# Optimization experiments

Measured on AMD Instinct MI355X. Metric: run time of the kernel, lower is better.

Reference implementation:

```python
import jax, jax.numpy as jnp
import numpy as np

B, S, D, H = 4, 2048, 1024, 16
DK = D // H


def setup_inputs() -> dict:
    key = jax.random.key(0)
    ks = jax.random.split(key, 5)
    init_std = np.sqrt(2.0 / (D + D))  # trunc bound proxy; plain randn clamped below
    trunc = 3 * init_std

    def w(k):
        return jnp.clip(jax.random.normal(k, (D, D), dtype=jnp.float32), -trunc, trunc)

    x = jax.random.normal(ks[0], (B, S, D), dtype=jnp.float32)
    return {
        "x": x,
        "W_Q": w(ks[1]),
        "W_K": w(ks[2]),
        "W_V": w(ks[3]),
        "W_O": w(ks[4]),
        "is_causal": 1,
    }


def reference(x, W_Q, W_K, W_V, W_O, is_causal):
    b, s, d = x.shape
    # Linear: y = W @ x with W:[out,in], x:[..., in]
    def proj(W, t):
        y = jnp.einsum("oi,bsi->bso", W, t)
        # [b, s, h*dk] -> [b, h, s, dk]
        return y.reshape(b, s, H, DK).transpose(0, 2, 1, 3)

    q = proj(W_Q, x)
    k = proj(W_K, x)
    v = proj(W_V, x)

    scores = jnp.einsum("bhqd,bhkd->bhqk", q, k) * (DK ** -0.5)
    if is_causal:
        causal = jnp.tril(jnp.ones((s, s), dtype=bool))
        scores = jnp.where(causal, scores, -jnp.inf)
    attn = jax.nn.softmax(scores, axis=-1)
    out = jnp.einsum("bhqk,bhkd->bhqd", attn, v)
    out = out.transpose(0, 2, 1, 3).reshape(b, s, H * DK)
    return jnp.einsum("oi,bsi->bso", W_O, out)
```

## Files before the change

### kernel.cpp

```cpp
#include <hip/hip_runtime.h>
#include <stdint.h>

#define NB 4
#define NS 2048
#define ND 1024
#define NH 16
#define NDK 64
#define L2E 1.44269504088896340736f
#define AS1 __attribute__((address_space(1)))
#define AS3 __attribute__((address_space(3)))

typedef __attribute__((ext_vector_type(8)))  short     s16x8;
typedef __attribute__((ext_vector_type(4)))  float     f32x4;
typedef __attribute__((ext_vector_type(16))) float     f32x16;
typedef __attribute__((ext_vector_type(4)))  unsigned  u32x4;

__device__ __forceinline__ unsigned short f2bf(float f) {
    union { float f; unsigned u; } v; v.f = f;
    unsigned r = v.u + 0x7FFFu + ((v.u >> 16) & 1u);
    return (unsigned short)(r >> 16);
}
__device__ __forceinline__ unsigned cvt_pk_bf16(float lo, float hi) {
    unsigned r;
    asm("v_cvt_pk_bf16_f32 %0, %1, %2" : "=v"(r) : "v"(lo), "v"(hi));
    return r;
}
__device__ __forceinline__ void pl32swap(unsigned &a, unsigned &b) {
    asm volatile("v_permlane32_swap_b32 %0, %1" : "+v"(a), "+v"(b));
}
__device__ __forceinline__ float exp2_hw(float x) {
    float r; asm("v_exp_f32 %0, %1" : "=v"(r) : "v"(x)); return r;
}
__device__ __forceinline__ f32x16 fz16() {
    f32x16 z;
#pragma unroll
    for (int r = 0; r < 16; ++r) z[r] = 0.f;
    return z;
}
__device__ __forceinline__ f32x16 mfma32(const s16x8& a, const s16x8& b, const f32x16& c) {
    return __builtin_amdgcn_mfma_f32_32x32x16_bf16(a, b, c, 0, 0, 0);
}

__global__ void detect_dtype(const unsigned* __restrict__ x, int* __restrict__ flag) {
    int lane = threadIdx.x;
    int cnt = 0;
    for (int i = lane; i < 1024; i += 64) {
        unsigned lo = x[i] & 0xFFFFu;
        unsigned e  = (lo >> 7) & 0xFFu;
        cnt += (e >= 100u && e <= 140u) ? 1 : 0;
    }
    for (int d = 1; d < 64; d <<= 1) cnt += __shfl_xor(cnt, d);
    if (lane == 0) flag[0] = (cnt > 512) ? 1 : 0;
}

__global__ void convert_all(const void* __restrict__ x,  const void* __restrict__ wq,
                            const void* __restrict__ wk, const void* __restrict__ wv,
                            unsigned short* __restrict__ XB, unsigned short* __restrict__ WQKV,
                            const int* __restrict__ flagp) {
    const int A  = (NB * NS * ND) / 8;
    const int WC = (ND * ND) / 8;
    int fl = *flagp;
    int i = blockIdx.x * blockDim.x + threadIdx.x;
    int stride = gridDim.x * blockDim.x;
    int total = A + 3 * WC;
    for (; i < total; i += stride) {
        const void* src; unsigned short* dst; long o8;
        if (i < A) { src = x; dst = XB; o8 = i; }
        else {
            int k = i - A, which = k >> 17, o = k & (WC - 1);
            src = which == 0 ? wq : (which == 1 ? wk : wv);
            dst = WQKV + (long)which * (ND * ND);
            o8 = o;
        }
        u32x4 v;
        if (fl) {
            v = *(const u32x4*)((const unsigned short*)src + o8 * 8);
        } else {
            const float* p = (const float*)src + o8 * 8;
            f32x4 a = *(const f32x4*)p;
            f32x4 b = *(const f32x4*)(p + 4);
            v[0] = cvt_pk_bf16(a[0], a[1]);
            v[1] = cvt_pk_bf16(a[2], a[3]);
            v[2] = cvt_pk_bf16(b[0], b[1]);
            v[3] = cvt_pk_bf16(b[2], b[3]);
        }
        *(u32x4*)(dst + o8 * 8) = v;
    }
}

__global__ void convert_bf16(const void* __restrict__ src, unsigned short* __restrict__ dst,
                             int n8, const int* __restrict__ flagp) {
    int i = blockIdx.x * blockDim.x + threadIdx.x;
    int stride = gridDim.x * blockDim.x;
    int fl = *flagp;
    for (; i < n8; i += stride) {
        u32x4 v;
        if (fl) {
            v = *(const u32x4*)((const unsigned short*)src + (long)i * 8);
        } else {
            const float* p = (const float*)src + (long)i * 8;
            f32x4 a = *(const f32x4*)p;
            f32x4 b = *(const f32x4*)(p + 4);
            v[0] = cvt_pk_bf16(a[0], a[1]);
            v[1] = cvt_pk_bf16(a[2], a[3]);
            v[2] = cvt_pk_bf16(b[0], b[1]);
            v[3] = cvt_pk_bf16(b[2], b[3]);
        }
        *(u32x4*)(dst + (long)i * 8) = v;
    }
}

__device__ __forceinline__ void stage_glds64(const unsigned short* __restrict__ src, int ld,
                                             long r0, int k0, unsigned short* lds, int tid) {
#pragma unroll
    for (int h = 0; h < 4; ++h) {
        int c = h * 256 + tid;
        int row = c >> 3;
        int scol = (c & 7) ^ (row & 7);
        const unsigned short* gp = src + (r0 + row) * ld + k0 + scol * 8;
        unsigned short* lp = lds + (c & ~63) * 8;
        __builtin_amdgcn_global_load_lds(
            (const AS1 unsigned short*)gp, (AS3 unsigned short*)lp, 16, 0, 0);
    }
}

template<int OUT_MODE, int NXB>
__global__ __launch_bounds__(256, 2)
void gemm3(const unsigned short* __restrict__ A, const unsigned short* __restrict__ W,
           void* __restrict__ dst, const int* __restrict__ flagp, float scale)
{
    __shared__ unsigned short As[128 * 64];
    __shared__ unsigned short Bs[128 * 64];
    const long TOKc = (long)NB * NS * ND;
    int tid  = threadIdx.x;
    int w    = tid >> 6, lane = tid & 63;
    int wr   = w >> 1,   wc   = w & 1;
    int nwg = (int)(gridDim.x * gridDim.y);
    int bid = (int)(blockIdx.y * gridDim.x + blockIdx.x);
    int nb  = (bid & 7) * (nwg >> 3) + (bid >> 3);
    int n0  = (nb % NXB) * 128;
    long m0 = (long)(nb / NXB) * 128;
    int fl  = *flagp;

    f32x4 zero4 = {0.f, 0.f, 0.f, 0.f};
    f32x4 acc[4][4];
#pragma unroll
    for (int i = 0; i < 4; ++i)
#pragma unroll
        for (int j = 0; j < 4; ++j) acc[i][j] = zero4;

    int lr = lane & 15, lg = lane >> 4;

    for (int k0 = 0; k0 < 1024; k0 += 64) {
        __syncthreads();
        stage_glds64(A, 1024, m0, k0, As, tid);
        stage_glds64(W, 1024, n0, k0, Bs, tid);
        __syncthreads();
#pragma unroll
        for (int kk = 0; kk < 2; ++kk) {
            s16x8 af[4], bf[4];
#pragma unroll
            for (int i = 0; i < 4; ++i) {
                int row = wr * 64 + i * 16 + lr;
                int u = (kk * 4 + lg) ^ (lr & 7);
                af[i] = *(const s16x8*)(As + row * 64 + u * 8);
            }
#pragma unroll
            for (int j = 0; j < 4; ++j) {
                int row = wc * 64 + j * 16 + lr;
                int u = (kk * 4 + lg) ^ (lr & 7);
                bf[j] = *(const s16x8*)(Bs + row * 64 + u * 8);
            }
#pragma unroll
            for (int i = 0; i < 4; ++i)
#pragma unroll
                for (int j = 0; j < 4; ++j)
                    acc[i][j] = __builtin_amdgcn_mfma_f32_16x16x32_bf16(af[i], bf[j], acc[i][j], 0, 0, 0);
        }
    }

    int rbase = (lane >> 4) * 4;
#pragma unroll
    for (int i = 0; i < 4; ++i)
#pragma unroll
        for (int j = 0; j < 4; ++j)
#pragma unroll
            for (int r = 0; r < 4; ++r) {
                long m = m0 + wr * 64 + i * 16 + rbase + r;
                int  n = n0 + wc * 64 + j * 16 + lr;
                float v = acc[i][j][r];
                if (OUT_MODE == 3) {
                    long b = m >> 11, s = m & 2047;
                    int hh = (n >> 6) & 15, dk = n & 63;
                    float sc = (n < 1024) ? scale : 1.0f;
                    long off = (n >= 1024) ? TOKc : 0;
                    ((unsigned short*)dst)[off + (((b * NH + hh) * NS) + s) * NDK + dk] = f2bf(v * sc);
                } else if (OUT_MODE == 1) {
                    int hh = (int)(m >> 6), dk = (int)(m & 63);
                    long b = n >> 11, s = n & 2047;
                    ((unsigned short*)dst)[(((b * NH + hh) * NDK) + dk) * NS + s] = f2bf(v * scale);
                } else {
                    if (fl) ((unsigned short*)dst)[m * 1024 + n] = f2bf(v * scale);
                    else    ((float*)dst)[m * 1024 + n] = v * scale;
                }
            }
}

__device__ __forceinline__ void stage_tile64(const char* __restrict__ srcbase, int rowstride,
                                             unsigned short* lds, int tid) {
#pragma unroll
    for (int h = 0; h < 2; ++h) {
        int c = h * 256 + tid;
        int L = c * 16;
        int row = L >> 7;
        int sr  = (L & 127) ^ ((row & 7) << 4);
        const char* gp = srcbase + row * rowstride + sr;
        unsigned short* lp = lds + (c & ~63) * 8;
        __builtin_amdgcn_global_load_lds((const AS1 unsigned short*)gp,
                                         (AS3 unsigned short*)lp, 16, 0, 0);
    }
}

__device__ __forceinline__ void sm64s(f32x16& st0, f32x16& st1, float& l,
                                      bool mask, int kv0, int qb, int l31, int hi,
                                      s16x8* pf)
{
    if (mask) {
        int q = qb + l31;
#pragma unroll
        for (int r = 0; r < 16; ++r) {
            int crow = (r & 3) + 8 * (r >> 2) + 4 * hi;
            if (kv0 + crow > q)      st0[r] = -1e30f;
            if (kv0 + 32 + crow > q) st1[r] = -1e30f;
        }
    }
#pragma unroll
    for (int r = 0; r < 16; ++r) {
        st0[r] = exp2_hw(st0[r]);
        st1[r] = exp2_hw(st1[r]);
    }
    float s8[8];
#pragma unroll
    for (int r = 0; r < 8; ++r) s8[r] = (st0[r] + st0[r + 8]) + (st1[r] + st1[r + 8]);
    float s4[4];
#pragma unroll
    for (int r = 0; r < 4; ++r) s4[r] = s8[r] + s8[r + 4];
    l += (s4[0] + s4[1]) + (s4[2] + s4[3]);

#pragma unroll
    for (int half = 0; half < 2; ++half) {
        const f32x16& st = half ? st1 : st0;
        unsigned b0 = cvt_pk_bf16(st[0],  st[1]);
        unsigned b1 = cvt_pk_bf16(st[2],  st[3]);
        unsigned b2 = cvt_pk_bf16(st[4],  st[5]);
        unsigned b3 = cvt_pk_bf16(st[6],  st[7]);
        unsigned b4 = cvt_pk_bf16(st[8],  st[9]);
        unsigned b5 = cvt_pk_bf16(st[10], st[11]);
        unsigned b6 = cvt_pk_bf16(st[12], st[13]);
        unsigned b7 = cvt_pk_bf16(st[14], st[15]);
        pl32swap(b0, b2);  pl32swap(b1, b3);
        pl32swap(b4, b6);  pl32swap(b5, b7);
        union { unsigned u[4]; s16x8 v; } p0, p1;
        p0.u[0] = b0; p0.u[1] = b1; p0.u[2] = b2; p0.u[3] = b3;
        p1.u[0] = b4; p1.u[1] = b5; p1.u[2] = b6; p1.u[3] = b7;
        pf[half * 2]     = p0.v;
        pf[half * 2 + 1] = p1.v;
    }
}

__device__ __forceinline__ void attn_epi(unsigned short* epb, const f32x16& o0, const f32x16& o1,
                                         float lrow, int l31, int hi, int lane,
                                         unsigned short* __restrict__ Oo, int qb, int b, int hh)
{
    float lt = lrow + __shfl_xor(lrow, 32);
    float inv = 1.0f / lt;
#pragma unroll
    for (int j = 0; j < 2; ++j) {
        const f32x16& o = j ? o1 : o0;
#pragma unroll
        for (int g = 0; g < 4; ++g) {
            int d0 = j * 32 + g * 8 + hi * 4;
            unsigned lo = cvt_pk_bf16(o[g * 4 + 0] * inv, o[g * 4 + 1] * inv);
            unsigned hw = cvt_pk_bf16(o[g * 4 + 2] * inv, o[g * 4 + 3] * inv);
            unsigned short* p = epb + l31 * 72 + d0;
            *(unsigned*)(p)     = lo;
            *(unsigned*)(p + 2) = hw;
        }
    }
    asm volatile("s_waitcnt lgkmcnt(0)" ::: "memory");
    __builtin_amdgcn_sched_barrier(0);
#pragma unroll
    for (int rr = 0; rr < 4; ++rr) {
        int q2 = rr * 8 + (lane >> 3);
        int d2 = (lane & 7) * 8;
        u32x4 vv = *(const u32x4*)(epb + q2 * 72 + d2);
        *(u32x4*)(Oo + (((long)b * NS + qb + q2) * ND) + hh * NDK + d2) = vv;
    }
}

__global__ __launch_bounds__(256, 3)
void attn_fwd11(const unsigned short* __restrict__ Q,
                const unsigned short* __restrict__ Kt,
                const unsigned short* __restrict__ Vt,
                unsigned short* __restrict__ Oo,
                const int* __restrict__ causalp)
{
    __shared__ char lds[2][16384];
    int tid = threadIdx.x, w = tid >> 6, lane = tid & 63;
    int l31 = lane & 31, hi = lane >> 5;
    int bh = blockIdx.x;
    int j  = 15 - (int)blockIdx.y;
    int t  = 4 * j + w, qb = t * 32;
    int causal = *causalp;
    int nst   = causal ? (2 * j + 2) : (NS / 64);
    int sdiag = causal ? (t >> 1) : 0x7FFFFFFF;

    const unsigned short* Qh = Q  + bh * (NS * NDK);
    const char* Khb = (const char*)(Kt + (long)bh * NS * NDK);
    const char* Vhb = (const char*)(Vt + (long)bh * NDK * NS);

    s16x8 qf[4];
#pragma unroll
    for (int kd = 0; kd < 4; ++kd)
        qf[kd] = *(const s16x8*)(Qh + (qb + l31) * NDK + kd * 16 + hi * 8);

    int koff[4];
#pragma unroll
    for (int kd = 0; kd < 4; ++kd)
        koff[kd] = l31 * 128 + ((kd * 32 + hi * 16) ^ ((l31 & 7) << 4));

    const f32x16 Z16 = fz16();
    f32x16 o0 = fz16(), o1 = fz16();
    float l = 0.f;

    stage_tile64(Khb, 128, (unsigned short*)&lds[0][0], tid);
    stage_tile64(Vhb, NS * 2, (unsigned short*)&lds[0][8192], tid);
    __syncthreads();

    int cur = 0;
    for (int s = 0; s < nst; ++s) {
        if (s + 1 < nst) {
            int kv1 = (s + 1) * 64;
            stage_tile64(Khb + (long)kv1 * 128, 128, (unsigned short*)&lds[cur ^ 1][0], tid);
            stage_tile64(Vhb + kv1 * 2, NS * 2, (unsigned short*)&lds[cur ^ 1][8192], tid);
        }
        if (s <= sdiag) {
            const char* kb = &lds[cur][0];
            const char* vb = &lds[cur][8192];
            f32x16 st0, st1;
            __builtin_amdgcn_s_setprio(1);
            {
                s16x8 k0 = *(const s16x8*)(kb + koff[0]);
                s16x8 k1 = *(const s16x8*)(kb + 4096 + koff[0]);
                st0 = mfma32(k0, qf[0], Z16);
                st1 = mfma32(k1, qf[0], Z16);
            }
#pragma unroll
            for (int kd = 1; kd < 4; ++kd) {
                s16x8 k0 = *(const s16x8*)(kb + koff[kd]);
                s16x8 k1 = *(const s16x8*)(kb + 4096 + koff[kd]);
                st0 = mfma32(k0, qf[kd], st0);
                st1 = mfma32(k1, qf[kd], st1);
            }
            __builtin_amdgcn_s_setprio(0);
            s16x8 pf[4];
            sm64s(st0, st1, l, s == sdiag, s * 64, qb, l31, hi, pf);
            __builtin_amdgcn_s_setprio(1);
#pragma unroll
            for (int ks = 0; ks < 4; ++ks) {
                s16x8 va = *(const s16x8*)(vb + koff[ks]);
                s16x8 wb = *(const s16x8*)(vb + 4096 + koff[ks]);
                o0 = mfma32(va, pf[ks], o0);
                o1 = mfma32(wb, pf[ks], o1);
            }
            __builtin_amdgcn_s_setprio(0);
        }
        __syncthreads();
        cur ^= 1;
    }

    unsigned short* ep = (unsigned short*)&lds[0][0] + w * (32 * 72);
    attn_epi(ep, o0, o1, l, l31, hi, lane, Oo, qb, bh >> 4, bh & 15);
}

extern "C" void kernel_launch(void* const* d_in, const int* in_sizes, int n_in,
                              void* d_out, int out_size, void* d_ws, size_t ws_size,
                              hipStream_t stream) {
    const void* x  = d_in[0];
    const void* Wq = d_in[1];
    const void* Wk = d_in[2];
    const void* Wv = d_in[3];
    const void* Wo = d_in[4];
    const int* causal = (const int*)d_in[5];

    const long TOK  = (long)NB * NS * ND;
    const long WTOK = (long)ND * ND;
    size_t need = 256 + 4UL * TOK * 2;
    if (ws_size < need) return;

    char* ws = (char*)d_ws;
    int* flag = (int*)ws;
    unsigned short* Qb = (unsigned short*)(ws + 256);
    unsigned short* Kb = Qb + TOK;
    unsigned short* Vb = Kb + TOK;
    unsigned short* XB = Vb + TOK;
    unsigned short* Ab = XB;
    unsigned short* WOB = Qb;
    unsigned short* WQKV = (unsigned short*)((char*)d_out + (size_t)out_size * 2 - 3UL * WTOK * 2);

    detect_dtype<<<1, 64, 0, stream>>>((const unsigned*)x, flag);
    convert_all<<<2048, 256, 0, stream>>>(x, Wq, Wk, Wv, XB, WQKV, flag);

    dim3 blk(256);
    gemm3<3, 16><<<dim3(16, 64), blk, 0, stream>>>(XB, WQKV, Qb, flag, 0.125f * L2E);
    gemm3<1, 64><<<dim3(64, 8), blk, 0, stream>>>(WQKV + 2 * WTOK, XB, Vb, flag, 1.0f);
    attn_fwd11<<<dim3(64, 16), blk, 0, stream>>>(Qb, Kb, Vb, Ab, causal);
    convert_bf16<<<512, 256, 0, stream>>>(Wo, WOB, (int)(WTOK / 8), flag);
    gemm3<2, 8><<<dim3(8, 64), blk, 0, stream>>>(Ab, WOB, d_out, flag, 1.0f);
}
```

Measured before the change: 156.4 us.

## Split causal attention into 2-wave blocks and fold dtype detection into conversion

The attention kernel now runs 128-thread blocks of two waves, each covering 64 query rows, and launches twice as many blocks along the query axis. Both waves in a block now need the same number of KV tiles, so the per-wave diagonal skip is removed and waves no longer sit idle while others finish. The cost is that each K/V tile staged in LDS is shared by fewer waves, so more tile loads per query row. Separately, the one-block dtype-detection kernel is merged into the conversion kernel, where every block repeats the small check, saving a launch.

```diff
diff --git a/kernel.cpp b/kernel.cpp
--- a/kernel.cpp
+++ b/kernel.cpp
@@ -41,26 +41,32 @@
     return __builtin_amdgcn_mfma_f32_32x32x16_bf16(a, b, c, 0, 0, 0);
 }
 
-__global__ void detect_dtype(const unsigned* __restrict__ x, int* __restrict__ flag) {
-    int lane = threadIdx.x;
-    int cnt = 0;
-    for (int i = lane; i < 1024; i += 64) {
-        unsigned lo = x[i] & 0xFFFFu;
-        unsigned e  = (lo >> 7) & 0xFFu;
-        cnt += (e >= 100u && e <= 140u) ? 1 : 0;
-    }
-    for (int d = 1; d < 64; d <<= 1) cnt += __shfl_xor(cnt, d);
-    if (lane == 0) flag[0] = (cnt > 512) ? 1 : 0;
-}
-
 __global__ void convert_all(const void* __restrict__ x,  const void* __restrict__ wq,
                             const void* __restrict__ wk, const void* __restrict__ wv,
                             unsigned short* __restrict__ XB, unsigned short* __restrict__ WQKV,
-                            const int* __restrict__ flagp) {
+                            int* __restrict__ flag) {
+    __shared__ int sfl;
+    int tid = threadIdx.x;
+    if (tid < 64) {
+        int cnt = 0;
+        const unsigned* xw = (const unsigned*)x;
+        for (int i = tid; i < 1024; i += 64) {
+            unsigned lo = xw[i] & 0xFFFFu;
+            unsigned e  = (lo >> 7) & 0xFFu;
+            cnt += (e >= 100u && e <= 140u) ? 1 : 0;
+        }
+        for (int d = 1; d < 64; d <<= 1) cnt += __shfl_xor(cnt, d);
+        if (tid == 0) {
+            sfl = (cnt > 512) ? 1 : 0;
+            if (blockIdx.x == 0) flag[0] = sfl;
+        }
+    }
+    __syncthreads();
+    int fl = sfl;
+
     const int A  = (NB * NS * ND) / 8;
     const int WC = (ND * ND) / 8;
-    int fl = *flagp;
-    int i = blockIdx.x * blockDim.x + threadIdx.x;
+    int i = blockIdx.x * blockDim.x + tid;
     int stride = gridDim.x * blockDim.x;
     int total = A + 3 * WC;
     for (; i < total; i += stride) {
@@ -209,8 +215,8 @@
 __device__ __forceinline__ void stage_tile64(const char* __restrict__ srcbase, int rowstride,
                                              unsigned short* lds, int tid) {
 #pragma unroll
-    for (int h = 0; h < 2; ++h) {
-        int c = h * 256 + tid;
+    for (int h = 0; h < 4; ++h) {
+        int c = h * 128 + tid;
         int L = c * 16;
         int row = L >> 7;
         int sr  = (L & 127) ^ ((row & 7) << 4);
@@ -298,8 +304,8 @@
     }
 }
 
-__global__ __launch_bounds__(256, 3)
-void attn_fwd11(const unsigned short* __restrict__ Q,
+__global__ __launch_bounds__(128)
+void attn_fwd12(const unsigned short* __restrict__ Q,
                 const unsigned short* __restrict__ Kt,
                 const unsigned short* __restrict__ Vt,
                 unsigned short* __restrict__ Oo,
@@ -309,10 +315,10 @@
     int tid = threadIdx.x, w = tid >> 6, lane = tid & 63;
     int l31 = lane & 31, hi = lane >> 5;
     int bh = blockIdx.x;
-    int j  = 15 - (int)blockIdx.y;
-    int t  = 4 * j + w, qb = t * 32;
+    int j  = 31 - (int)blockIdx.y;
+    int t  = 2 * j + w, qb = t * 32;
     int causal = *causalp;
-    int nst   = causal ? (2 * j + 2) : (NS / 64);
+    int nst   = causal ? (j + 1) : (NS / 64);
     int sdiag = causal ? (t >> 1) : 0x7FFFFFFF;
 
     const unsigned short* Qh = Q  + bh * (NS * NDK);
@@ -344,7 +350,7 @@
             stage_tile64(Khb + (long)kv1 * 128, 128, (unsigned short*)&lds[cur ^ 1][0], tid);
             stage_tile64(Vhb + kv1 * 2, NS * 2, (unsigned short*)&lds[cur ^ 1][8192], tid);
         }
-        if (s <= sdiag) {
+        {
             const char* kb = &lds[cur][0];
             const char* vb = &lds[cur][8192];
             f32x16 st0, st1;
@@ -408,13 +414,12 @@
     unsigned short* WOB = Qb;
     unsigned short* WQKV = (unsigned short*)((char*)d_out + (size_t)out_size * 2 - 3UL * WTOK * 2);
 
-    detect_dtype<<<1, 64, 0, stream>>>((const unsigned*)x, flag);
     convert_all<<<2048, 256, 0, stream>>>(x, Wq, Wk, Wv, XB, WQKV, flag);
 
     dim3 blk(256);
     gemm3<3, 16><<<dim3(16, 64), blk, 0, stream>>>(XB, WQKV, Qb, flag, 0.125f * L2E);
     gemm3<1, 64><<<dim3(64, 8), blk, 0, stream>>>(WQKV + 2 * WTOK, XB, Vb, flag, 1.0f);
-    attn_fwd11<<<dim3(64, 16), blk, 0, stream>>>(Qb, Kb, Vb, Ab, causal);
+    attn_fwd12<<<dim3(64, 32), 128, 0, stream>>>(Qb, Kb, Vb, Ab, causal);
     convert_bf16<<<512, 256, 0, stream>>>(Wo, WOB, (int)(WTOK / 8), flag);
     gemm3<2, 8><<<dim3(8, 64), blk, 0, stream>>>(Ab, WOB, d_out, flag, 1.0f);
 }
```

After: 166.1 us. +6.2%, slower.
